# Kernel optimization log

Hardware: AMD Instinct MI355X
Metric: run time of the kernel (lower is better)

The kernel has to match this reference:

```python
import jax, jax.numpy as jnp
import numpy as np

T, D, F, G, H = 364, 512, 28, 30000, 128
CIN = 2 * D + F + 1  # 1053


def setup_inputs() -> dict:
    key = jax.random.key(0)
    k = jax.random.split(key, 12)
    s = 0.02  # weight scale so activations stay in a sane range
    return {
        "emb_table": jax.random.normal(k[0], (T, D), jnp.float32),
        "Wp": jax.random.normal(k[1], (D, CIN), jnp.float32) * s,
        "bp": jnp.zeros((D,), jnp.float32),
        "W_ih": jax.random.normal(k[2], (3 * D, D), jnp.float32) * s,
        "b_ih": jnp.zeros((3 * D,), jnp.float32),
        "W_hh": jax.random.normal(k[3], (3 * D, D), jnp.float32) * s,
        "b_hh": jnp.zeros((3 * D,), jnp.float32),
        "ln_g": jnp.ones((D,), jnp.float32),
        "ln_b": jnp.zeros((D,), jnp.float32),
        "Wi1": jax.random.normal(k[4], (H, D), jnp.float32) * s,
        "bi1": jnp.zeros((H,), jnp.float32),
        "Wi2": jax.random.normal(k[5], (1, H), jnp.float32) * s,
        "bi2": jnp.zeros((1,), jnp.float32),
        "features_a": jax.random.normal(k[6], (G, F), jnp.float32),
        "features_b": jax.random.normal(k[7], (G, F), jnp.float32),
        "team_a": jax.random.randint(k[8], (G,), 0, T),
        "team_b": jax.random.randint(k[9], (G,), 0, T),
        "a_won": jax.random.randint(k[10], (G,), 0, 2),
    }


def reference(emb_table, Wp, bp, W_ih, b_ih, W_hh, b_hh, ln_g, ln_b,
              Wi1, bi1, Wi2, bi2, features_a, features_b,
              team_a, team_b, a_won):
    def step(emb, x):
        ta, tb, fa, fb, aw = x
        aw = aw.astype(jnp.float32)
        # both directions of the game processed together as a batch of 2
        e_self = jnp.stack([emb[ta], emb[tb]])                 # [2, D]
        e_opp = e_self[::-1]                                   # [2, D]
        won = jnp.stack([aw, 1.0 - aw])[:, None]               # [2, 1]
        comb = jnp.concatenate([e_self, e_opp, jnp.stack([fa, fb]), won], axis=-1)  # [2, CIN]
        proj = jax.nn.relu(comb @ Wp.T + bp)                   # dropout = identity (eval)
        imp = jax.nn.sigmoid(jax.nn.relu(proj @ Wi1.T + bi1) @ Wi2.T + bi2)  # [2, 1]
        # torch GRUCell
        gi = proj @ W_ih.T + b_ih                              # [2, 3D]
        gh = e_self @ W_hh.T + b_hh
        i_r, i_z, i_n = jnp.split(gi, 3, axis=-1)
        h_r, h_z, h_n = jnp.split(gh, 3, axis=-1)
        r = jax.nn.sigmoid(i_r + h_r)
        z = jax.nn.sigmoid(i_z + h_z)
        n = jnp.tanh(i_n + r * h_n)
        new_h = (1.0 - z) * n + z * e_self
        upd = e_self + imp * (new_h - e_self)
        # LayerNorm(eps=1e-5)
        mu = jnp.mean(upd, axis=-1, keepdims=True)
        var = jnp.mean((upd - mu) ** 2, axis=-1, keepdims=True)
        upd = (upd - mu) / jnp.sqrt(var + 1e-5) * ln_g + ln_b
        emb = emb.at[ta].set(upd[0]).at[tb].set(upd[1])
        return emb, jax.lax.stop_gradient(proj)                # game_context is detached

    final_emb, contexts = jax.lax.scan(
        step, emb_table, (team_a, team_b, features_a, features_b, a_won))
    return final_emb, contexts  # [T, D], [G, 2, D]
```

## Files before the change

kernel.cpp:

```cpp
#include <hip/hip_runtime.h>
#include <math.h>


#define NG   30000
#define NT   364
#define ND   512
#define NF   28
#define NH   128
#define NCIN 1053
#define NB   256
#define BLK  1024
#define WCAP 192

__device__ __forceinline__ float sigmf(float x) { return 1.0f / (1.0f + expf(-x)); }

__device__ __forceinline__ void astore_f(float* p, float v) {
  __hip_atomic_store(p, v, __ATOMIC_RELAXED, __HIP_MEMORY_SCOPE_AGENT);
}
__device__ __forceinline__ void astore_f2(float* p, float x, float y) {
  float2 v = make_float2(x, y);
  unsigned long long u; __builtin_memcpy(&u, &v, 8);
  __hip_atomic_store((unsigned long long*)p, u, __ATOMIC_RELAXED, __HIP_MEMORY_SCOPE_AGENT);
}

__global__ void zero_kernel(int* p, int n) {
  int i = blockIdx.x * blockDim.x + threadIdx.x;
  if (i < n) p[i] = 0;
}

__global__ void deps_kernel(const int* __restrict__ ta, const int* __restrict__ tb,
                            int* __restrict__ dep0, int* __restrict__ dep1) {
  int g = blockIdx.x * blockDim.x + threadIdx.x;
  if (g >= NG) return;
  int a = ta[g], b = tb[g];
  int d0 = -1, d1 = -1;
  for (int p = g - 1; p >= 0; --p) {
    int pa = ta[p], pb = tb[p];
    if (d0 < 0 && (pa == a || pb == a)) d0 = p;
    if (d1 < 0 && (pa == b || pb == b)) d1 = p;
    if (d0 >= 0 && d1 >= 0) break;
  }
  dep0[g] = d0;
  dep1[g] = d1;
}

__global__ void levels_kernel(const int* __restrict__ d0a, const int* __restrict__ d1a,
                              int* __restrict__ level, int* __restrict__ nLevels) {
  __shared__ int lv[1024];
  __shared__ int changed;
  __shared__ int smax;
  const int tid = threadIdx.x;
  int localMax = 0;
  if (tid == 0) smax = 0;
  for (int base = 0; base < NG; base += 1024) {
    const int g = base + tid;
    const bool val = g < NG;
    int ic0 = -1, ic1 = -1, b = 0;
    if (val) {
      int d0 = d0a[g], d1 = d1a[g];
      if (d0 >= 0) { if (d0 < base) b = max(b, level[d0] + 1); else ic0 = d0 - base; }
      if (d1 >= 0) { if (d1 < base) b = max(b, level[d1] + 1); else ic1 = d1 - base; }
    }
    lv[tid] = b;
    __syncthreads();
    for (;;) {
      if (tid == 0) changed = 0;
      __syncthreads();
      int nl = lv[tid];
      if (ic0 >= 0) nl = max(nl, lv[ic0] + 1);
      if (ic1 >= 0) nl = max(nl, lv[ic1] + 1);
      if (val && nl != lv[tid]) { lv[tid] = nl; changed = 1; }
      __syncthreads();
      if (!changed) break;
    }
    if (val) { level[g] = lv[tid]; localMax = max(localMax, lv[tid]); }
    __syncthreads();
  }
  atomicMax(&smax, localMax);
  __syncthreads();
  if (tid == 0) nLevels[0] = smax + 1;
}

__global__ void sort_kernel(const int* __restrict__ level, const int* __restrict__ nLevels,
                            int* __restrict__ hist, int* __restrict__ cursor,
                            int* __restrict__ levelStart, int* __restrict__ levelList) {
  const int tid = threadIdx.x;
  const int nL = nLevels[0];
  for (int i = tid; i < NG; i += 1024) { hist[i] = 0; cursor[i] = 0; }
  __syncthreads();
  for (int g = tid; g < NG; g += 1024) atomicAdd(&hist[level[g]], 1);
  __syncthreads();
  if (tid == 0) {
    int acc = 0;
    for (int i = 0; i < nL; ++i) { levelStart[i] = acc; acc += hist[i]; }
    levelStart[nL] = acc;
  }
  __syncthreads();
  for (int g = tid; g < NG; g += 1024) {
    int l = level[g];
    int off = atomicAdd(&cursor[l], 1);
    levelList[levelStart[l] + off] = g;
  }
}

__device__ __forceinline__ void grid_bar(int* go, int* arr, int& epoch) {
  ++epoch;
  __syncthreads();
  if (blockIdx.x == 0) {
    const int t = threadIdx.x;
    if (t >= 1 && t < NB) {
      while (__hip_atomic_load(arr + t * 32, __ATOMIC_RELAXED, __HIP_MEMORY_SCOPE_AGENT) < epoch)
        __builtin_amdgcn_s_sleep(1);
    }
    __builtin_amdgcn_fence(__ATOMIC_ACQUIRE, "agent");
    __syncthreads();
    if (t == 0)
      __hip_atomic_store(go, epoch, __ATOMIC_RELEASE, __HIP_MEMORY_SCOPE_AGENT);
  } else {
    if (threadIdx.x == 0) {
      __hip_atomic_store(arr + blockIdx.x * 32, epoch, __ATOMIC_RELEASE, __HIP_MEMORY_SCOPE_AGENT);
      while (__hip_atomic_load(go, __ATOMIC_RELAXED, __HIP_MEMORY_SCOPE_AGENT) < epoch)
        __builtin_amdgcn_s_sleep(1);
      __builtin_amdgcn_fence(__ATOMIC_ACQUIRE, "agent");
    }
    __syncthreads();
  }
}

__global__ __launch_bounds__(BLK, 4)
void game_kernel(const float* __restrict__ Wp,   const float* __restrict__ bp,
                 const float* __restrict__ W_ih, const float* __restrict__ b_ih,
                 const float* __restrict__ W_hh, const float* __restrict__ b_hh,
                 const float* __restrict__ ln_g, const float* __restrict__ ln_b,
                 const float* __restrict__ Wi1,  const float* __restrict__ bi1,
                 const float* __restrict__ Wi2,  const float* __restrict__ bi2,
                 const float* __restrict__ fA,   const float* __restrict__ fB,
                 const int* __restrict__ team_a, const int* __restrict__ team_b,
                 const int* __restrict__ a_won,
                 float* __restrict__ emb, float* __restrict__ ctx,
                 const int* __restrict__ levelStart, const int* __restrict__ levelList,
                 const int* __restrict__ nLevels,
                 float* __restrict__ nhbuf, float* __restrict__ hidbuf,
                 int* __restrict__ go, int* __restrict__ arr, int Wcap) {
  const int b    = blockIdx.x;
  const int tid  = threadIdx.x;
  const int lane = tid & 63;
  const int wave = tid >> 6;
  const int grpq = lane >> 4;
  const int l4   = lane & 15;
  const int d0   = 2 * b;
  const int r_b  = b >> 7;
  const int h_b  = b & 127;

  __shared__ float4 wpS4[256];
  __shared__ float4 wpO4[256];
  __shared__ float2 wpT2[32];
  __shared__ float4 wih4[768];
  __shared__ float4 whh4[768];
  __shared__ float2 wi12[256];
  __shared__ float4 sStash[WCAP][4];
  __shared__ float sImp[2];
  __shared__ float sRed[2][16];
  __shared__ float sStat[4];

  if (tid < 256) {
    const int p = tid;
    wpS4[p] = make_float4(Wp[(size_t)d0 * NCIN + 2 * p],
                          Wp[(size_t)(d0 + 1) * NCIN + 2 * p],
                          Wp[(size_t)d0 * NCIN + 2 * p + 1],
                          Wp[(size_t)(d0 + 1) * NCIN + 2 * p + 1]);
    wpO4[p] = make_float4(Wp[(size_t)d0 * NCIN + ND + 2 * p],
                          Wp[(size_t)(d0 + 1) * NCIN + ND + 2 * p],
                          Wp[(size_t)d0 * NCIN + ND + 2 * p + 1],
                          Wp[(size_t)(d0 + 1) * NCIN + ND + 2 * p + 1]);
    wi12[p] = make_float2(Wi1[(size_t)h_b * ND + 2 * p],
                          Wi1[(size_t)h_b * ND + 2 * p + 1]);
  } else if (tid < 288) {
    const int t = tid - 256;
    wpT2[t] = (t < NF + 1)
        ? make_float2(Wp[(size_t)d0 * NCIN + 2 * ND + t],
                      Wp[(size_t)(d0 + 1) * NCIN + 2 * ND + t])
        : make_float2(0.f, 0.f);
  }
  if (tid < 768) {
    const int gt = tid >> 8, p = tid & 255;
    wih4[tid] = make_float4(W_ih[((size_t)gt * ND + d0) * ND + 2 * p],
                            W_ih[((size_t)gt * ND + d0 + 1) * ND + 2 * p],
                            W_ih[((size_t)gt * ND + d0) * ND + 2 * p + 1],
                            W_ih[((size_t)gt * ND + d0 + 1) * ND + 2 * p + 1]);
    whh4[tid] = make_float4(W_hh[((size_t)gt * ND + d0) * ND + 2 * p],
                            W_hh[((size_t)gt * ND + d0 + 1) * ND + 2 * p],
                            W_hh[((size_t)gt * ND + d0) * ND + 2 * p + 1],
                            W_hh[((size_t)gt * ND + d0 + 1) * ND + 2 * p + 1]);
  }

  const float bp0 = bp[d0], bp1 = bp[d0 + 1];
  float bih[6], bhh[6];
#pragma unroll
  for (int gt = 0; gt < 3; ++gt)
#pragma unroll
    for (int d = 0; d < 2; ++d) {
      bih[gt * 2 + d] = b_ih[gt * ND + d0 + d];
      bhh[gt * 2 + d] = b_hh[gt * ND + d0 + d];
    }
  const float bi1h = bi1[h_b];
  const float bi2v = bi2[0];
  const float2 w2p = ((const float2*)Wi2)[lane];
  float2 lg2 = make_float2(0.f, 0.f), lb2 = lg2;
  if (tid < 512) {
    lg2 = ((const float2*)ln_g)[tid & 255];
    lb2 = ((const float2*)ln_b)[tid & 255];
  }
  __syncthreads();

  const int nL = nLevels[0];
  int epoch = 0;

  for (int L = 0; L < nL; ++L) {
    const int s = levelStart[L], e_ = levelStart[L + 1];
    for (int cs = s; cs < e_; cs += Wcap) {
      const int W = min(e_ - cs, Wcap);

      for (int w = wave * 4 + grpq; w < W; w += 64) {
        const int g = levelList[cs + w];
        const int ta = team_a[g], tb = team_b[g];
        const float aw = (float)a_won[g];
        const float* rowA = emb + (size_t)ta * ND;
        const float* rowB = emb + (size_t)tb * ND;
        float acc[16];
#pragma unroll
        for (int i = 0; i < 16; ++i) acc[i] = 0.f;
#pragma unroll 4
        for (int j = 0; j < 16; ++j) {
          const int p = j * 16 + l4;
          const float2 va = *(const float2*)(rowA + 2 * p);
          const float2 vb = *(const float2*)(rowB + 2 * p);
          const float4 wS = wpS4[p];
          const float4 wO = wpO4[p];
          acc[0] += va.x * wS.x + va.y * wS.z + vb.x * wO.x + vb.y * wO.z;
          acc[1] += va.x * wS.y + va.y * wS.w + vb.x * wO.y + vb.y * wO.w;
          acc[2] += vb.x * wS.x + vb.y * wS.z + va.x * wO.x + va.y * wO.z;
          acc[3] += vb.x * wS.y + vb.y * wS.w + va.x * wO.y + va.y * wO.w;
#pragma unroll
          for (int gt = 0; gt < 3; ++gt) {
            const float4 q = whh4[gt * 256 + p];
            acc[4 + gt * 2 + 0]  += va.x * q.x + va.y * q.z;
            acc[4 + gt * 2 + 1]  += va.x * q.y + va.y * q.w;
            acc[10 + gt * 2 + 0] += vb.x * q.x + vb.y * q.z;
            acc[10 + gt * 2 + 1] += vb.x * q.y + vb.y * q.w;
          }
        }
#pragma unroll
        for (int j = 0; j < 2; ++j) {
          const int t = j * 16 + l4;
          if (t < NF + 1) {
            const float cv0 = (t < NF) ? fA[(size_t)g * NF + t] : aw;
            const float cv1 = (t < NF) ? fB[(size_t)g * NF + t] : 1.0f - aw;
            const float2 wt = wpT2[t];
            acc[0] += cv0 * wt.x; acc[1] += cv0 * wt.y;
            acc[2] += cv1 * wt.x; acc[3] += cv1 * wt.y;
          }
        }
#pragma unroll
        for (int off = 8; off > 0; off >>= 1) {
#pragma unroll
          for (int i = 0; i < 16; ++i) acc[i] += __shfl_xor(acc[i], off);
        }
        if (l4 == 0) {
          astore_f2(ctx + (size_t)g * 1024 + d0,
                    fmaxf(acc[0] + bp0, 0.f), fmaxf(acc[1] + bp1, 0.f));
          astore_f2(ctx + (size_t)g * 1024 + ND + d0,
                    fmaxf(acc[2] + bp0, 0.f), fmaxf(acc[3] + bp1, 0.f));
          const float2 es0 = *(const float2*)(rowA + d0);
          const float2 es1 = *(const float2*)(rowB + d0);
          sStash[w][0] = make_float4(acc[4], acc[5], acc[6], acc[7]);
          sStash[w][1] = make_float4(acc[8], acc[9], es0.x, es0.y);
          sStash[w][2] = make_float4(acc[10], acc[11], acc[12], acc[13]);
          sStash[w][3] = make_float4(acc[14], acc[15], es1.x, es1.y);
        }
      }
      grid_bar(go, arr, epoch);

      for (int w = wave * 4 + grpq; w < W; w += 64) {
        const int g = levelList[cs + w];
        const float* p0 = ctx + (size_t)g * 1024;
        const float* p1 = p0 + ND;
        float acc[13];
#pragma unroll
        for (int i = 0; i < 13; ++i) acc[i] = 0.f;
#pragma unroll 4
        for (int j = 0; j < 16; ++j) {
          const int p = j * 16 + l4;
          const float2 x0 = *(const float2*)(p0 + 2 * p);
          const float2 x1 = *(const float2*)(p1 + 2 * p);
#pragma unroll
          for (int gt = 0; gt < 3; ++gt) {
            const float4 q = wih4[gt * 256 + p];
            acc[gt * 2 + 0]     += x0.x * q.x + x0.y * q.z;
            acc[gt * 2 + 1]     += x0.x * q.y + x0.y * q.w;
            acc[6 + gt * 2 + 0] += x1.x * q.x + x1.y * q.z;
            acc[6 + gt * 2 + 1] += x1.x * q.y + x1.y * q.w;
          }
          const float2 wi = wi12[p];
          const float2 xr = r_b ? x1 : x0;
          acc[12] += xr.x * wi.x + xr.y * wi.y;
        }
#pragma unroll
        for (int off = 8; off > 0; off >>= 1) {
#pragma unroll
          for (int i = 0; i < 13; ++i) acc[i] += __shfl_xor(acc[i], off);
        }
        if (l4 == 0) {
          const float4 s0 = sStash[w][0], s1 = sStash[w][1];
          const float4 s2 = sStash[w][2], s3 = sStash[w][3];
          {
            const float r0 = sigmf(acc[0] + bih[0] + s0.x + bhh[0]);
            const float r1 = sigmf(acc[1] + bih[1] + s0.y + bhh[1]);
            const float z0 = sigmf(acc[2] + bih[2] + s0.z + bhh[2]);
            const float z1 = sigmf(acc[3] + bih[3] + s0.w + bhh[3]);
            const float n0 = tanhf(acc[4] + bih[4] + r0 * (s1.x + bhh[4]));
            const float n1 = tanhf(acc[5] + bih[5] + r1 * (s1.y + bhh[5]));
            astore_f2(nhbuf + (size_t)w * 1024 + d0,
                      (1.f - z0) * n0 + z0 * s1.z,
                      (1.f - z1) * n1 + z1 * s1.w);
          }
          {
            const float r0 = sigmf(acc[6] + bih[0] + s2.x + bhh[0]);
            const float r1 = sigmf(acc[7] + bih[1] + s2.y + bhh[1]);
            const float z0 = sigmf(acc[8] + bih[2] + s2.z + bhh[2]);
            const float z1 = sigmf(acc[9] + bih[3] + s2.w + bhh[3]);
            const float n0 = tanhf(acc[10] + bih[4] + r0 * (s3.x + bhh[4]));
            const float n1 = tanhf(acc[11] + bih[5] + r1 * (s3.y + bhh[5]));
            astore_f2(nhbuf + (size_t)w * 1024 + ND + d0,
                      (1.f - z0) * n0 + z0 * s3.z,
                      (1.f - z1) * n1 + z1 * s3.w);
          }
          astore_f(hidbuf + (size_t)w * 256 + r_b * NH + h_b,
                   fmaxf(acc[12] + bi1h, 0.f));
        }
      }
      grid_bar(go, arr, epoch);

      for (int w = b; w < W; w += NB) {
        const int g = levelList[cs + w];
        const int ta = team_a[g], tb = team_b[g];
        if (wave < 2) {
          const float2 hv = *(const float2*)(hidbuf + (size_t)w * 256 + wave * NH + 2 * lane);
          float a = hv.x * w2p.x + hv.y * w2p.y;
#pragma unroll
          for (int off = 32; off > 0; off >>= 1) a += __shfl_xor(a, off);
          if (lane == 0) sImp[wave] = sigmf(a + bi2v);
        }
        __syncthreads();
        float ux = 0.f, uy = 0.f;
        if (tid < 512) {
          const int row = tid >> 8;
          const int e = 2 * (tid & 255);
          const int team = row ? tb : ta;
          const float imp = sImp[row];
          const float2 ev = *(const float2*)(emb + (size_t)team * ND + e);
          const float2 nv = *(const float2*)(nhbuf + (size_t)w * 1024 + (size_t)row * ND + e);
          ux = ev.x + imp * (nv.x - ev.x);
          uy = ev.y + imp * (nv.y - ev.y);
        }
        float sS = ux + uy, sQ = ux * ux + uy * uy;
#pragma unroll
        for (int off = 32; off > 0; off >>= 1) {
          sS += __shfl_xor(sS, off);
          sQ += __shfl_xor(sQ, off);
        }
        if (lane == 0) { sRed[0][wave] = sS; sRed[1][wave] = sQ; }
        __syncthreads();
        if (tid == 0) {
          const float S0 = sRed[0][0] + sRed[0][1] + sRed[0][2] + sRed[0][3];
          const float Q0 = sRed[1][0] + sRed[1][1] + sRed[1][2] + sRed[1][3];
          const float S1 = sRed[0][4] + sRed[0][5] + sRed[0][6] + sRed[0][7];
          const float Q1 = sRed[1][4] + sRed[1][5] + sRed[1][6] + sRed[1][7];
          const float mu0 = S0 * (1.0f / ND), mu1 = S1 * (1.0f / ND);
          const float v0 = Q0 * (1.0f / ND) - mu0 * mu0;
          const float v1 = Q1 * (1.0f / ND) - mu1 * mu1;
          sStat[0] = mu0; sStat[1] = 1.0f / sqrtf(v0 + 1e-5f);
          sStat[2] = mu1; sStat[3] = 1.0f / sqrtf(v1 + 1e-5f);
        }
        __syncthreads();
        if (tid < 512) {
          const int row = tid >> 8;
          const int e = 2 * (tid & 255);
          const float mu = sStat[row * 2], rs = sStat[row * 2 + 1];
          const float ox = (ux - mu) * rs * lg2.x + lb2.x;
          const float oy = (uy - mu) * rs * lg2.y + lb2.y;
          if (row == 0) {
            if (ta != tb) astore_f2(emb + (size_t)ta * ND + e, ox, oy);
          } else {
            astore_f2(emb + (size_t)tb * ND + e, ox, oy);
          }
        }
        __syncthreads();
      }
      grid_bar(go, arr, epoch);
    }
  }
}

extern "C" void kernel_launch(void* const* d_in, const int* in_sizes, int n_in,
                              void* d_out, int out_size, void* d_ws, size_t ws_size,
                              hipStream_t stream) {
  const float* emb_table = (const float*)d_in[0];
  const float* Wp    = (const float*)d_in[1];
  const float* bp    = (const float*)d_in[2];
  const float* W_ih  = (const float*)d_in[3];
  const float* b_ih  = (const float*)d_in[4];
  const float* W_hh  = (const float*)d_in[5];
  const float* b_hh  = (const float*)d_in[6];
  const float* ln_g  = (const float*)d_in[7];
  const float* ln_b  = (const float*)d_in[8];
  const float* Wi1   = (const float*)d_in[9];
  const float* bi1   = (const float*)d_in[10];
  const float* Wi2   = (const float*)d_in[11];
  const float* bi2   = (const float*)d_in[12];
  const float* fA    = (const float*)d_in[13];
  const float* fB    = (const float*)d_in[14];
  const int*   team_a = (const int*)d_in[15];
  const int*   team_b = (const int*)d_in[16];
  const int*   a_won  = (const int*)d_in[17];

  float* out = (float*)d_out;
  float* emb = out;
  float* ctx = out + (size_t)NT * ND;

  int* ip         = (int*)d_ws;
  int* go         = ip;
  int* arr        = ip + 32;
  int* nLevels    = ip + 32 + NB * 32;
  int* dep0       = nLevels + 32;
  int* dep1       = dep0 + NG;
  int* level      = dep1 + NG;
  int* hist       = level + NG;
  int* cursor     = hist + NG;
  int* levelStart = cursor + NG;
  int* levelList  = levelStart + NG + 2;
  const int flagInts = 32 + NB * 32;
  size_t control = (size_t)((char*)(levelList + NG) - (char*)d_ws);
  control = (control + 255) & ~(size_t)255;

  int Wcap = WCAP;
  {
    size_t avail = (ws_size > control + 4096)
        ? (ws_size - control) / ((size_t)(1024 + 256) * sizeof(float))
        : 8;
    if (avail < (size_t)Wcap) Wcap = (int)avail;
    if (Wcap < 8) Wcap = 8;
  }
  float* nhbuf  = (float*)((char*)d_ws + control);
  float* hidbuf = nhbuf + (size_t)Wcap * 1024;

  hipMemcpyAsync(emb, emb_table, (size_t)NT * ND * sizeof(float),
                 hipMemcpyDeviceToDevice, stream);
  zero_kernel<<<(flagInts + 255) / 256, 256, 0, stream>>>(ip, flagInts);
  deps_kernel<<<(NG + 255) / 256, 256, 0, stream>>>(team_a, team_b, dep0, dep1);
  levels_kernel<<<1, 1024, 0, stream>>>(dep0, dep1, level, nLevels);
  sort_kernel<<<1, 1024, 0, stream>>>(level, nLevels, hist, cursor, levelStart, levelList);
  game_kernel<<<NB, BLK, 0, stream>>>(
      Wp, bp, W_ih, b_ih, W_hh, b_hh, ln_g, ln_b, Wi1, bi1, Wi2, bi2,
      fA, fB, team_a, team_b, a_won, emb, ctx,
      levelStart, levelList, nLevels, nhbuf, hidbuf, go, arr, Wcap);
}
```

Before: 23.91 ms.

## Split feature dims across 512 blocks and replicate grid-barrier release flags

Doubles the persistent grid from 256 to 512 blocks, so each block owns one output feature instead of two. This halves per-block shared weights, accumulators and work per level. The self-embedding element is now taken from the main loop through a shuffle reduction instead of a separate load. The grid barrier now publishes the release epoch to 8 replicated flags and spins without sleep, to cut contention from more waiters. The cost is that the 512 co-resident blocks need launch bounds of 8 per CU and the barrier gathers from twice as many arrivals.

Measured after the change: 52.45 ms. 2.19x slower.

```diff
diff --git a/kernel.cpp b/kernel.cpp
--- a/kernel.cpp
+++ b/kernel.cpp
@@ -8,7 +8,7 @@
 #define NF   28
 #define NH   128
 #define NCIN 1053
-#define NB   256
+#define NB   512
 #define BLK  1024
 #define WCAP 192
 
@@ -103,7 +103,7 @@
   }
 }
 
-__device__ __forceinline__ void grid_bar(int* go, int* arr, int& epoch) {
+__device__ __forceinline__ void grid_bar(int* goRep, int* arr, int& epoch) {
   ++epoch;
   __syncthreads();
   if (blockIdx.x == 0) {
@@ -114,20 +114,20 @@
     }
     __builtin_amdgcn_fence(__ATOMIC_ACQUIRE, "agent");
     __syncthreads();
-    if (t == 0)
-      __hip_atomic_store(go, epoch, __ATOMIC_RELEASE, __HIP_MEMORY_SCOPE_AGENT);
+    if (t < 8)
+      __hip_atomic_store(goRep + t * 32, epoch, __ATOMIC_RELEASE, __HIP_MEMORY_SCOPE_AGENT);
   } else {
     if (threadIdx.x == 0) {
       __hip_atomic_store(arr + blockIdx.x * 32, epoch, __ATOMIC_RELEASE, __HIP_MEMORY_SCOPE_AGENT);
-      while (__hip_atomic_load(go, __ATOMIC_RELAXED, __HIP_MEMORY_SCOPE_AGENT) < epoch)
-        __builtin_amdgcn_s_sleep(1);
+      int* goMine = goRep + (blockIdx.x & 7) * 32;
+      while (__hip_atomic_load(goMine, __ATOMIC_RELAXED, __HIP_MEMORY_SCOPE_AGENT) < epoch) { }
       __builtin_amdgcn_fence(__ATOMIC_ACQUIRE, "agent");
     }
     __syncthreads();
   }
 }
 
-__global__ __launch_bounds__(BLK, 4)
+__global__ __launch_bounds__(BLK, 8)
 void game_kernel(const float* __restrict__ Wp,   const float* __restrict__ bp,
                  const float* __restrict__ W_ih, const float* __restrict__ b_ih,
                  const float* __restrict__ W_hh, const float* __restrict__ b_hh,
@@ -141,68 +141,55 @@
                  const int* __restrict__ levelStart, const int* __restrict__ levelList,
                  const int* __restrict__ nLevels,
                  float* __restrict__ nhbuf, float* __restrict__ hidbuf,
-                 int* __restrict__ go, int* __restrict__ arr, int Wcap) {
+                 int* __restrict__ goRep, int* __restrict__ arr, int Wcap) {
   const int b    = blockIdx.x;
   const int tid  = threadIdx.x;
   const int lane = tid & 63;
   const int wave = tid >> 6;
   const int grpq = lane >> 4;
   const int l4   = lane & 15;
-  const int d0   = 2 * b;
-  const int r_b  = b >> 7;
+  const int d0   = b;
+  const int r_b  = (b >> 7) & 1;
   const int h_b  = b & 127;
 
-  __shared__ float4 wpS4[256];
-  __shared__ float4 wpO4[256];
-  __shared__ float2 wpT2[32];
-  __shared__ float4 wih4[768];
-  __shared__ float4 whh4[768];
+  __shared__ float2 wpS2[256];
+  __shared__ float2 wpO2[256];
+  __shared__ float  wpT1[32];
+  __shared__ float2 wih2[768];
+  __shared__ float2 whh2[768];
   __shared__ float2 wi12[256];
-  __shared__ float4 sStash[WCAP][4];
+  __shared__ float4 sStash[WCAP][2];
   __shared__ float sImp[2];
   __shared__ float sRed[2][16];
   __shared__ float sStat[4];
 
   if (tid < 256) {
     const int p = tid;
-    wpS4[p] = make_float4(Wp[(size_t)d0 * NCIN + 2 * p],
-                          Wp[(size_t)(d0 + 1) * NCIN + 2 * p],
-                          Wp[(size_t)d0 * NCIN + 2 * p + 1],
-                          Wp[(size_t)(d0 + 1) * NCIN + 2 * p + 1]);
-    wpO4[p] = make_float4(Wp[(size_t)d0 * NCIN + ND + 2 * p],
-                          Wp[(size_t)(d0 + 1) * NCIN + ND + 2 * p],
-                          Wp[(size_t)d0 * NCIN + ND + 2 * p + 1],
-                          Wp[(size_t)(d0 + 1) * NCIN + ND + 2 * p + 1]);
+    wpS2[p] = make_float2(Wp[(size_t)d0 * NCIN + 2 * p],
+                          Wp[(size_t)d0 * NCIN + 2 * p + 1]);
+    wpO2[p] = make_float2(Wp[(size_t)d0 * NCIN + ND + 2 * p],
+                          Wp[(size_t)d0 * NCIN + ND + 2 * p + 1]);
     wi12[p] = make_float2(Wi1[(size_t)h_b * ND + 2 * p],
                           Wi1[(size_t)h_b * ND + 2 * p + 1]);
   } else if (tid < 288) {
     const int t = tid - 256;
-    wpT2[t] = (t < NF + 1)
-        ? make_float2(Wp[(size_t)d0 * NCIN + 2 * ND + t],
-                      Wp[(size_t)(d0 + 1) * NCIN + 2 * ND + t])
-        : make_float2(0.f, 0.f);
+    wpT1[t] = (t < NF + 1) ? Wp[(size_t)d0 * NCIN + 2 * ND + t] : 0.f;
   }
   if (tid < 768) {
     const int gt = tid >> 8, p = tid & 255;
-    wih4[tid] = make_float4(W_ih[((size_t)gt * ND + d0) * ND + 2 * p],
-                            W_ih[((size_t)gt * ND + d0 + 1) * ND + 2 * p],
-                            W_ih[((size_t)gt * ND + d0) * ND + 2 * p + 1],
-                            W_ih[((size_t)gt * ND + d0 + 1) * ND + 2 * p + 1]);
-    whh4[tid] = make_float4(W_hh[((size_t)gt * ND + d0) * ND + 2 * p],
-                            W_hh[((size_t)gt * ND + d0 + 1) * ND + 2 * p],
-                            W_hh[((size_t)gt * ND + d0) * ND + 2 * p + 1],
-                            W_hh[((size_t)gt * ND + d0 + 1) * ND + 2 * p + 1]);
-  }
-
-  const float bp0 = bp[d0], bp1 = bp[d0 + 1];
-  float bih[6], bhh[6];
-#pragma unroll
-  for (int gt = 0; gt < 3; ++gt)
-#pragma unroll
-    for (int d = 0; d < 2; ++d) {
-      bih[gt * 2 + d] = b_ih[gt * ND + d0 + d];
-      bhh[gt * 2 + d] = b_hh[gt * ND + d0 + d];
-    }
+    wih2[tid] = make_float2(W_ih[((size_t)gt * ND + d0) * ND + 2 * p],
+                            W_ih[((size_t)gt * ND + d0) * ND + 2 * p + 1]);
+    whh2[tid] = make_float2(W_hh[((size_t)gt * ND + d0) * ND + 2 * p],
+                            W_hh[((size_t)gt * ND + d0) * ND + 2 * p + 1]);
+  }
+
+  const float bp0 = bp[d0];
+  float bih[3], bhh[3];
+#pragma unroll
+  for (int gt = 0; gt < 3; ++gt) {
+    bih[gt] = b_ih[gt * ND + d0];
+    bhh[gt] = b_hh[gt * ND + d0];
+  }
   const float bi1h = bi1[h_b];
   const float bi2v = bi2[0];
   const float2 w2p = ((const float2*)Wi2)[lane];
@@ -215,6 +202,8 @@
 
   const int nL = nLevels[0];
   int epoch = 0;
+  const int pairD = d0 >> 1;
+  const int elemD = d0 & 1;
 
   for (int L = 0; L < nL; ++L) {
     const int s = levelStart[L], e_ = levelStart[L + 1];
@@ -227,27 +216,28 @@
         const float aw = (float)a_won[g];
         const float* rowA = emb + (size_t)ta * ND;
         const float* rowB = emb + (size_t)tb * ND;
-        float acc[16];
-#pragma unroll
-        for (int i = 0; i < 16; ++i) acc[i] = 0.f;
+        float acc[8];
+#pragma unroll
+        for (int i = 0; i < 8; ++i) acc[i] = 0.f;
+        float es0 = 0.f, es1 = 0.f;
 #pragma unroll 4
         for (int j = 0; j < 16; ++j) {
           const int p = j * 16 + l4;
           const float2 va = *(const float2*)(rowA + 2 * p);
           const float2 vb = *(const float2*)(rowB + 2 * p);
-          const float4 wS = wpS4[p];
-          const float4 wO = wpO4[p];
-          acc[0] += va.x * wS.x + va.y * wS.z + vb.x * wO.x + vb.y * wO.z;
-          acc[1] += va.x * wS.y + va.y * wS.w + vb.x * wO.y + vb.y * wO.w;
-          acc[2] += vb.x * wS.x + vb.y * wS.z + va.x * wO.x + va.y * wO.z;
-          acc[3] += vb.x * wS.y + vb.y * wS.w + va.x * wO.y + va.y * wO.w;
+          const float2 wS = wpS2[p];
+          const float2 wO = wpO2[p];
+          acc[0] += va.x * wS.x + va.y * wS.y + vb.x * wO.x + vb.y * wO.y;
+          acc[1] += vb.x * wS.x + vb.y * wS.y + va.x * wO.x + va.y * wO.y;
 #pragma unroll
           for (int gt = 0; gt < 3; ++gt) {
-            const float4 q = whh4[gt * 256 + p];
-            acc[4 + gt * 2 + 0]  += va.x * q.x + va.y * q.z;
-            acc[4 + gt * 2 + 1]  += va.x * q.y + va.y * q.w;
-            acc[10 + gt * 2 + 0] += vb.x * q.x + vb.y * q.z;
-            acc[10 + gt * 2 + 1] += vb.x * q.y + vb.y * q.w;
+            const float2 q = whh2[gt * 256 + p];
+            acc[2 + gt] += va.x * q.x + va.y * q.y;
+            acc[5 + gt] += vb.x * q.x + vb.y * q.y;
+          }
+          if (p == pairD) {
+            es0 = elemD ? va.y : va.x;
+            es1 = elemD ? vb.y : vb.x;
           }
         }
 #pragma unroll
@@ -256,38 +246,34 @@
           if (t < NF + 1) {
             const float cv0 = (t < NF) ? fA[(size_t)g * NF + t] : aw;
             const float cv1 = (t < NF) ? fB[(size_t)g * NF + t] : 1.0f - aw;
-            const float2 wt = wpT2[t];
-            acc[0] += cv0 * wt.x; acc[1] += cv0 * wt.y;
-            acc[2] += cv1 * wt.x; acc[3] += cv1 * wt.y;
+            const float wt = wpT1[t];
+            acc[0] += cv0 * wt;
+            acc[1] += cv1 * wt;
           }
         }
 #pragma unroll
         for (int off = 8; off > 0; off >>= 1) {
 #pragma unroll
-          for (int i = 0; i < 16; ++i) acc[i] += __shfl_xor(acc[i], off);
+          for (int i = 0; i < 8; ++i) acc[i] += __shfl_xor(acc[i], off);
+          es0 += __shfl_xor(es0, off);
+          es1 += __shfl_xor(es1, off);
         }
         if (l4 == 0) {
-          astore_f2(ctx + (size_t)g * 1024 + d0,
-                    fmaxf(acc[0] + bp0, 0.f), fmaxf(acc[1] + bp1, 0.f));
-          astore_f2(ctx + (size_t)g * 1024 + ND + d0,
-                    fmaxf(acc[2] + bp0, 0.f), fmaxf(acc[3] + bp1, 0.f));
-          const float2 es0 = *(const float2*)(rowA + d0);
-          const float2 es1 = *(const float2*)(rowB + d0);
-          sStash[w][0] = make_float4(acc[4], acc[5], acc[6], acc[7]);
-          sStash[w][1] = make_float4(acc[8], acc[9], es0.x, es0.y);
-          sStash[w][2] = make_float4(acc[10], acc[11], acc[12], acc[13]);
-          sStash[w][3] = make_float4(acc[14], acc[15], es1.x, es1.y);
+          astore_f(ctx + (size_t)g * 1024 + d0, fmaxf(acc[0] + bp0, 0.f));
+          astore_f(ctx + (size_t)g * 1024 + ND + d0, fmaxf(acc[1] + bp0, 0.f));
+          sStash[w][0] = make_float4(acc[2], acc[3], acc[4], es0);
+          sStash[w][1] = make_float4(acc[5], acc[6], acc[7], es1);
         }
       }
-      grid_bar(go, arr, epoch);
+      grid_bar(goRep, arr, epoch);
 
       for (int w = wave * 4 + grpq; w < W; w += 64) {
         const int g = levelList[cs + w];
         const float* p0 = ctx + (size_t)g * 1024;
         const float* p1 = p0 + ND;
-        float acc[13];
-#pragma unroll
-        for (int i = 0; i < 13; ++i) acc[i] = 0.f;
+        float acc[7];
+#pragma unroll
+        for (int i = 0; i < 7; ++i) acc[i] = 0.f;
 #pragma unroll 4
         for (int j = 0; j < 16; ++j) {
           const int p = j * 16 + l4;
@@ -295,51 +281,38 @@
           const float2 x1 = *(const float2*)(p1 + 2 * p);
 #pragma unroll
           for (int gt = 0; gt < 3; ++gt) {
-            const float4 q = wih4[gt * 256 + p];
-            acc[gt * 2 + 0]     += x0.x * q.x + x0.y * q.z;
-            acc[gt * 2 + 1]     += x0.x * q.y + x0.y * q.w;
-            acc[6 + gt * 2 + 0] += x1.x * q.x + x1.y * q.z;
-            acc[6 + gt * 2 + 1] += x1.x * q.y + x1.y * q.w;
+            const float2 q = wih2[gt * 256 + p];
+            acc[gt]     += x0.x * q.x + x0.y * q.y;
+            acc[3 + gt] += x1.x * q.x + x1.y * q.y;
           }
           const float2 wi = wi12[p];
           const float2 xr = r_b ? x1 : x0;
-          acc[12] += xr.x * wi.x + xr.y * wi.y;
+          acc[6] += xr.x * wi.x + xr.y * wi.y;
         }
 #pragma unroll
         for (int off = 8; off > 0; off >>= 1) {
 #pragma unroll
-          for (int i = 0; i < 13; ++i) acc[i] += __shfl_xor(acc[i], off);
+          for (int i = 0; i < 7; ++i) acc[i] += __shfl_xor(acc[i], off);
         }
         if (l4 == 0) {
           const float4 s0 = sStash[w][0], s1 = sStash[w][1];
-          const float4 s2 = sStash[w][2], s3 = sStash[w][3];
           {
-            const float r0 = sigmf(acc[0] + bih[0] + s0.x + bhh[0]);
-            const float r1 = sigmf(acc[1] + bih[1] + s0.y + bhh[1]);
-            const float z0 = sigmf(acc[2] + bih[2] + s0.z + bhh[2]);
-            const float z1 = sigmf(acc[3] + bih[3] + s0.w + bhh[3]);
-            const float n0 = tanhf(acc[4] + bih[4] + r0 * (s1.x + bhh[4]));
-            const float n1 = tanhf(acc[5] + bih[5] + r1 * (s1.y + bhh[5]));
-            astore_f2(nhbuf + (size_t)w * 1024 + d0,
-                      (1.f - z0) * n0 + z0 * s1.z,
-                      (1.f - z1) * n1 + z1 * s1.w);
+            const float r = sigmf(acc[0] + bih[0] + s0.x + bhh[0]);
+            const float z = sigmf(acc[1] + bih[1] + s0.y + bhh[1]);
+            const float n = tanhf(acc[2] + bih[2] + r * (s0.z + bhh[2]));
+            astore_f(nhbuf + (size_t)w * 1024 + d0, (1.f - z) * n + z * s0.w);
           }
           {
-            const float r0 = sigmf(acc[6] + bih[0] + s2.x + bhh[0]);
-            const float r1 = sigmf(acc[7] + bih[1] + s2.y + bhh[1]);
-            const float z0 = sigmf(acc[8] + bih[2] + s2.z + bhh[2]);
-            const float z1 = sigmf(acc[9] + bih[3] + s2.w + bhh[3]);
-            const float n0 = tanhf(acc[10] + bih[4] + r0 * (s3.x + bhh[4]));
-            const float n1 = tanhf(acc[11] + bih[5] + r1 * (s3.y + bhh[5]));
-            astore_f2(nhbuf + (size_t)w * 1024 + ND + d0,
-                      (1.f - z0) * n0 + z0 * s3.z,
-                      (1.f - z1) * n1 + z1 * s3.w);
+            const float r = sigmf(acc[3] + bih[0] + s1.x + bhh[0]);
+            const float z = sigmf(acc[4] + bih[1] + s1.y + bhh[1]);
+            const float n = tanhf(acc[5] + bih[2] + r * (s1.z + bhh[2]));
+            astore_f(nhbuf + (size_t)w * 1024 + ND + d0, (1.f - z) * n + z * s1.w);
           }
           astore_f(hidbuf + (size_t)w * 256 + r_b * NH + h_b,
-                   fmaxf(acc[12] + bi1h, 0.f));
+                   fmaxf(acc[6] + bi1h, 0.f));
         }
       }
-      grid_bar(go, arr, epoch);
+      grid_bar(goRep, arr, epoch);
 
       for (int w = b; w < W; w += NB) {
         const int g = levelList[cs + w];
@@ -397,7 +370,7 @@
         }
         __syncthreads();
       }
-      grid_bar(go, arr, epoch);
+      grid_bar(goRep, arr, epoch);
     }
   }
 }
@@ -429,9 +402,9 @@
   float* ctx = out + (size_t)NT * ND;
 
   int* ip         = (int*)d_ws;
-  int* go         = ip;
-  int* arr        = ip + 32;
-  int* nLevels    = ip + 32 + NB * 32;
+  int* goRep      = ip;
+  int* arr        = ip + 256;
+  int* nLevels    = ip + 256 + NB * 32;
   int* dep0       = nLevels + 32;
   int* dep1       = dep0 + NG;
   int* level      = dep1 + NG;
@@ -439,7 +412,7 @@
   int* cursor     = hist + NG;
   int* levelStart = cursor + NG;
   int* levelList  = levelStart + NG + 2;
-  const int flagInts = 32 + NB * 32;
+  const int flagInts = 256 + NB * 32;
   size_t control = (size_t)((char*)(levelList + NG) - (char*)d_ws);
   control = (control + 255) & ~(size_t)255;
 
@@ -463,5 +436,5 @@
   game_kernel<<<NB, BLK, 0, stream>>>(
       Wp, bp, W_ih, b_ih, W_hh, b_hh, ln_g, ln_b, Wi1, bi1, Wi2, bi2,
       fA, fB, team_a, team_b, a_won, emb, ctx,
-      levelStart, levelList, nLevels, nhbuf, hidbuf, go, arr, Wcap);
-}
+      levelStart, levelList, nLevels, nhbuf, hidbuf, goRep, arr, Wcap);
+}
```

## Replace master-block grid barrier with all-poll flags and single-wave LayerNorm update

Applied to the files above, without the earlier changes.

The grid barrier no longer has block 0 gather arrivals and release a go flag. Each block now writes its own epoch flag and its first wave polls all 256 flags directly, removing one round-trip of cross-block signalling per barrier. The third phase (importance, blend, LayerNorm, embedding write) now runs on a single wave per block, with each half-wave handling one team row using register reductions instead of block-wide shared-memory reductions and several __syncthreads. In exchange, every block polls 256 flags, which adds memory traffic while waiting, and each block now handles only game w=b, assuming W ≤ NB.

Result: slower. 73.98 ms (+209.4%).

```diff
diff --git a/kernel.cpp b/kernel.cpp
--- a/kernel.cpp
+++ b/kernel.cpp
@@ -103,28 +103,24 @@
   }
 }
 
-__device__ __forceinline__ void grid_bar(int* go, int* arr, int& epoch) {
+__device__ __forceinline__ void grid_bar(int* arr, int& epoch) {
   ++epoch;
   __syncthreads();
-  if (blockIdx.x == 0) {
-    const int t = threadIdx.x;
-    if (t >= 1 && t < NB) {
-      while (__hip_atomic_load(arr + t * 32, __ATOMIC_RELAXED, __HIP_MEMORY_SCOPE_AGENT) < epoch)
-        __builtin_amdgcn_s_sleep(1);
+  if (threadIdx.x == 0)
+    __hip_atomic_store(arr + blockIdx.x * 32, epoch, __ATOMIC_RELEASE, __HIP_MEMORY_SCOPE_AGENT);
+  if (threadIdx.x < 64) {
+    const int i0 = threadIdx.x, i1 = i0 + 64, i2 = i0 + 128, i3 = i0 + 192;
+    for (;;) {
+      const int v0 = __hip_atomic_load(arr + i0 * 32, __ATOMIC_RELAXED, __HIP_MEMORY_SCOPE_AGENT);
+      const int v1 = __hip_atomic_load(arr + i1 * 32, __ATOMIC_RELAXED, __HIP_MEMORY_SCOPE_AGENT);
+      const int v2 = __hip_atomic_load(arr + i2 * 32, __ATOMIC_RELAXED, __HIP_MEMORY_SCOPE_AGENT);
+      const int v3 = __hip_atomic_load(arr + i3 * 32, __ATOMIC_RELAXED, __HIP_MEMORY_SCOPE_AGENT);
+      if (min(min(v0, v1), min(v2, v3)) >= epoch) break;
+      __builtin_amdgcn_s_sleep(2);
     }
-    __builtin_amdgcn_fence(__ATOMIC_ACQUIRE, "agent");
-    __syncthreads();
-    if (t == 0)
-      __hip_atomic_store(go, epoch, __ATOMIC_RELEASE, __HIP_MEMORY_SCOPE_AGENT);
-  } else {
-    if (threadIdx.x == 0) {
-      __hip_atomic_store(arr + blockIdx.x * 32, epoch, __ATOMIC_RELEASE, __HIP_MEMORY_SCOPE_AGENT);
-      while (__hip_atomic_load(go, __ATOMIC_RELAXED, __HIP_MEMORY_SCOPE_AGENT) < epoch)
-        __builtin_amdgcn_s_sleep(1);
-      __builtin_amdgcn_fence(__ATOMIC_ACQUIRE, "agent");
-    }
-    __syncthreads();
-  }
+  }
+  __builtin_amdgcn_fence(__ATOMIC_ACQUIRE, "agent");
+  __syncthreads();
 }
 
 __global__ __launch_bounds__(BLK, 4)
@@ -141,13 +137,15 @@
                  const int* __restrict__ levelStart, const int* __restrict__ levelList,
                  const int* __restrict__ nLevels,
                  float* __restrict__ nhbuf, float* __restrict__ hidbuf,
-                 int* __restrict__ go, int* __restrict__ arr, int Wcap) {
+                 int* __restrict__ arr, int Wcap) {
   const int b    = blockIdx.x;
   const int tid  = threadIdx.x;
   const int lane = tid & 63;
   const int wave = tid >> 6;
   const int grpq = lane >> 4;
   const int l4   = lane & 15;
+  const int half = lane >> 5;
+  const int l5   = lane & 31;
   const int d0   = 2 * b;
   const int r_b  = b >> 7;
   const int h_b  = b & 127;
@@ -159,9 +157,6 @@
   __shared__ float4 whh4[768];
   __shared__ float2 wi12[256];
   __shared__ float4 sStash[WCAP][4];
-  __shared__ float sImp[2];
-  __shared__ float sRed[2][16];
-  __shared__ float sStat[4];
 
   if (tid < 256) {
     const int p = tid;
@@ -205,11 +200,13 @@
     }
   const float bi1h = bi1[h_b];
   const float bi2v = bi2[0];
-  const float2 w2p = ((const float2*)Wi2)[lane];
-  float2 lg2 = make_float2(0.f, 0.f), lb2 = lg2;
-  if (tid < 512) {
-    lg2 = ((const float2*)ln_g)[tid & 255];
-    lb2 = ((const float2*)ln_b)[tid & 255];
+  const float2 w2r0 = ((const float2*)Wi2)[l5];
+  const float2 w2r1 = ((const float2*)Wi2)[32 + l5];
+  float2 lng2[8], lnb2[8];
+#pragma unroll
+  for (int j = 0; j < 8; ++j) {
+    lng2[j] = ((const float2*)ln_g)[j * 32 + l5];
+    lnb2[j] = ((const float2*)ln_b)[j * 32 + l5];
   }
   __syncthreads();
 
@@ -279,7 +276,7 @@
           sStash[w][3] = make_float4(acc[14], acc[15], es1.x, es1.y);
         }
       }
-      grid_bar(go, arr, epoch);
+      grid_bar(arr, epoch);
 
       for (int w = wave * 4 + grpq; w < W; w += 64) {
         const int g = levelList[cs + w];
@@ -339,65 +336,58 @@
                    fmaxf(acc[12] + bi1h, 0.f));
         }
       }
-      grid_bar(go, arr, epoch);
-
-      for (int w = b; w < W; w += NB) {
-        const int g = levelList[cs + w];
+      grid_bar(arr, epoch);
+
+      if (wave == 0 && b < W) {
+        const int w = b;
+        const int g  = levelList[cs + w];
         const int ta = team_a[g], tb = team_b[g];
-        if (wave < 2) {
-          const float2 hv = *(const float2*)(hidbuf + (size_t)w * 256 + wave * NH + 2 * lane);
-          float a = hv.x * w2p.x + hv.y * w2p.y;
-#pragma unroll
-          for (int off = 32; off > 0; off >>= 1) a += __shfl_xor(a, off);
-          if (lane == 0) sImp[wave] = sigmf(a + bi2v);
-        }
-        __syncthreads();
-        float ux = 0.f, uy = 0.f;
-        if (tid < 512) {
-          const int row = tid >> 8;
-          const int e = 2 * (tid & 255);
-          const int team = row ? tb : ta;
-          const float imp = sImp[row];
-          const float2 ev = *(const float2*)(emb + (size_t)team * ND + e);
-          const float2 nv = *(const float2*)(nhbuf + (size_t)w * 1024 + (size_t)row * ND + e);
-          ux = ev.x + imp * (nv.x - ev.x);
-          uy = ev.y + imp * (nv.y - ev.y);
-        }
-        float sS = ux + uy, sQ = ux * ux + uy * uy;
-#pragma unroll
-        for (int off = 32; off > 0; off >>= 1) {
+        const int team = half ? tb : ta;
+        const float* ep = emb + (size_t)team * ND;
+        const float* np = nhbuf + (size_t)w * 1024 + (size_t)half * ND;
+        const float* hp = hidbuf + (size_t)w * 256 + half * NH;
+        const float2 h20 = *(const float2*)(hp + 2 * l5);
+        const float2 h21 = *(const float2*)(hp + 2 * (32 + l5));
+        float2 e2[8], n2[8];
+#pragma unroll
+        for (int j = 0; j < 8; ++j) {
+          const int p = j * 32 + l5;
+          e2[j] = *(const float2*)(ep + 2 * p);
+          n2[j] = *(const float2*)(np + 2 * p);
+        }
+        float ip = h20.x * w2r0.x + h20.y * w2r0.y + h21.x * w2r1.x + h21.y * w2r1.y;
+#pragma unroll
+        for (int off = 16; off > 0; off >>= 1) ip += __shfl_xor(ip, off);
+        ip = sigmf(ip + bi2v);
+        float sS = 0.f, sQ = 0.f;
+#pragma unroll
+        for (int j = 0; j < 8; ++j) {
+          const float ux = e2[j].x + ip * (n2[j].x - e2[j].x);
+          const float uy = e2[j].y + ip * (n2[j].y - e2[j].y);
+          sS += ux + uy;
+          sQ += ux * ux + uy * uy;
+        }
+#pragma unroll
+        for (int off = 16; off > 0; off >>= 1) {
           sS += __shfl_xor(sS, off);
           sQ += __shfl_xor(sQ, off);
         }
-        if (lane == 0) { sRed[0][wave] = sS; sRed[1][wave] = sQ; }
-        __syncthreads();
-        if (tid == 0) {
-          const float S0 = sRed[0][0] + sRed[0][1] + sRed[0][2] + sRed[0][3];
-          const float Q0 = sRed[1][0] + sRed[1][1] + sRed[1][2] + sRed[1][3];
-          const float S1 = sRed[0][4] + sRed[0][5] + sRed[0][6] + sRed[0][7];
-          const float Q1 = sRed[1][4] + sRed[1][5] + sRed[1][6] + sRed[1][7];
-          const float mu0 = S0 * (1.0f / ND), mu1 = S1 * (1.0f / ND);
-          const float v0 = Q0 * (1.0f / ND) - mu0 * mu0;
-          const float v1 = Q1 * (1.0f / ND) - mu1 * mu1;
-          sStat[0] = mu0; sStat[1] = 1.0f / sqrtf(v0 + 1e-5f);
-          sStat[2] = mu1; sStat[3] = 1.0f / sqrtf(v1 + 1e-5f);
-        }
-        __syncthreads();
-        if (tid < 512) {
-          const int row = tid >> 8;
-          const int e = 2 * (tid & 255);
-          const float mu = sStat[row * 2], rs = sStat[row * 2 + 1];
-          const float ox = (ux - mu) * rs * lg2.x + lb2.x;
-          const float oy = (uy - mu) * rs * lg2.y + lb2.y;
-          if (row == 0) {
-            if (ta != tb) astore_f2(emb + (size_t)ta * ND + e, ox, oy);
-          } else {
-            astore_f2(emb + (size_t)tb * ND + e, ox, oy);
-          }
-        }
-        __syncthreads();
+        const float mu = sS * (1.0f / ND);
+        const float var = sQ * (1.0f / ND) - mu * mu;
+        const float rstd = 1.0f / sqrtf(var + 1e-5f);
+        if (half == 1 || ta != tb) {
+#pragma unroll
+          for (int j = 0; j < 8; ++j) {
+            const int p = j * 32 + l5;
+            const float ux = e2[j].x + ip * (n2[j].x - e2[j].x);
+            const float uy = e2[j].y + ip * (n2[j].y - e2[j].y);
+            astore_f2(emb + (size_t)team * ND + 2 * p,
+                      (ux - mu) * rstd * lng2[j].x + lnb2[j].x,
+                      (uy - mu) * rstd * lng2[j].y + lnb2[j].y);
+          }
+        }
       }
-      grid_bar(go, arr, epoch);
+      grid_bar(arr, epoch);
     }
   }
 }
@@ -429,9 +419,8 @@
   float* ctx = out + (size_t)NT * ND;
 
   int* ip         = (int*)d_ws;
-  int* go         = ip;
-  int* arr        = ip + 32;
-  int* nLevels    = ip + 32 + NB * 32;
+  int* arr        = ip;
+  int* nLevels    = ip + NB * 32;
   int* dep0       = nLevels + 32;
   int* dep1       = dep0 + NG;
   int* level      = dep1 + NG;
@@ -439,7 +428,7 @@
   int* cursor     = hist + NG;
   int* levelStart = cursor + NG;
   int* levelList  = levelStart + NG + 2;
-  const int flagInts = 32 + NB * 32;
+  const int flagInts = NB * 32;
   size_t control = (size_t)((char*)(levelList + NG) - (char*)d_ws);
   control = (control + 255) & ~(size_t)255;
 
@@ -463,5 +452,5 @@
   game_kernel<<<NB, BLK, 0, stream>>>(
       Wp, bp, W_ih, b_ih, W_hh, b_hh, ln_g, ln_b, Wi1, bi1, Wi2, bi2,
       fA, fB, team_a, team_b, a_won, emb, ctx,
-      levelStart, levelList, nLevels, nhbuf, hidbuf, go, arr, Wcap);
-}
+      levelStart, levelList, nLevels, nhbuf, hidbuf, arr, Wcap);
+}
```
